# Kernel optimization log

Hardware: AMD Instinct MI355X
Metric: run time of the kernel (lower is better)

Reference implementation:

```python
import jax, jax.numpy as jnp
import numpy as np
from jax import lax

N, L = 4000, 128          # total sentences, sentence length
VOCAB = 50002             # 50000 words + unk + blk
VEC_DIM, POS_DIM = 50, 5
EMB = VEC_DIM + 2 * POS_DIM   # 60
HID = 230
NPOS = 201                # 2*max_pos_length+1
NBAG, BAGSZ = 500, 8
NREL = 25


def setup_inputs() -> dict:
    key = jax.random.key(0)
    ks = jax.random.split(key, 10)
    X = jax.random.randint(ks[0], (N, L), 0, 50000)
    pos1 = jax.random.randint(ks[1], (N, L), 0, NPOS)
    pos2 = jax.random.randint(ks[2], (N, L), 0, NPOS)
    mask = jnp.zeros((N, L), dtype=jnp.int64)       # unused by CNN encoder
    length = jnp.full((N,), L, dtype=jnp.int64)     # unused by CNN encoder
    starts = jnp.arange(NBAG) * BAGSZ
    scope = jnp.stack([starts, starts + BAGSZ], axis=1)  # [NBAG, 2] contiguous bags
    relation = jax.random.randint(ks[3], (NBAG,), 0, NREL)
    word_emb = jax.random.normal(ks[4], (VOCAB, VEC_DIM), jnp.float32) * 0.1
    pos1_emb = jax.random.normal(ks[5], (NPOS, POS_DIM), jnp.float32) * 0.1
    pos2_emb = jax.random.normal(ks[6], (NPOS, POS_DIM), jnp.float32) * 0.1
    conv_w = jax.random.normal(ks[7], (HID, EMB, 3), jnp.float32) * (1.0 / np.sqrt(EMB * 3))
    conv_b = jnp.zeros((HID,), jnp.float32)
    rel_w = jax.random.normal(ks[8], (NREL, HID), jnp.float32) * (1.0 / np.sqrt(HID))
    rel_b = jnp.zeros((NREL,), jnp.float32)
    return {"X": X, "pos1": pos1, "pos2": pos2, "mask": mask, "length": length,
            "scope": scope, "relation": relation, "word_emb": word_emb,
            "pos1_emb": pos1_emb, "pos2_emb": pos2_emb, "conv_w": conv_w,
            "conv_b": conv_b, "rel_w": rel_w, "rel_b": rel_b}


def reference(X, pos1, pos2, mask, length, scope, relation,
              word_emb, pos1_emb, pos2_emb, conv_w, conv_b, rel_w, rel_b):
    # --- word_pos_embedding: gather + concat -> [N, L, EMB]
    emb = jnp.concatenate([word_emb[X], pos1_emb[pos1], pos2_emb[pos2]], axis=-1)
    # --- CNN encoder: conv1d(k=3, same pad) -> max-pool over seq -> relu
    h = lax.conv_general_dilated(
        emb.transpose(0, 2, 1), conv_w, window_strides=(1,), padding='SAME',
        dimension_numbers=('NCH', 'OIH', 'NCH'))  # [N, HID, L]
    h = jax.nn.relu(jnp.max(h + conv_b[None, :, None], axis=2))  # [N, HID]
    # (dropout p=0.0 -> identity)
    # --- ragged per-bag softmax attention pooling (training path, relation given)
    sizes = scope[:, 1] - scope[:, 0]
    bag_ids = jnp.repeat(jnp.arange(NBAG), sizes, total_repeat_length=N)  # [N]
    rel_q = rel_w[relation]                       # [NBAG, HID] attention queries
    logits = jnp.sum(h * rel_q[bag_ids], axis=-1)  # [N]
    m = jax.ops.segment_max(logits, bag_ids, num_segments=NBAG)
    e = jnp.exp(logits - m[bag_ids])
    denom = jax.ops.segment_sum(e, bag_ids, num_segments=NBAG)
    alpha = e / denom[bag_ids]                     # per-bag softmax weights
    bag_rep = jax.ops.segment_sum(alpha[:, None] * h, bag_ids, num_segments=NBAG)  # [NBAG, HID]
    # --- relation classifier
    return bag_rep @ rel_w.T + rel_b               # [NBAG, NREL]
```

## Files before the change

### kernel.cpp

```cpp
#include <hip/hip_runtime.h>
#include <hip/hip_bf16.h>

#define NSENT 4000
#define LSEQ  128
#define VEC   50
#define POS   5
#define EMBD  60
#define HIDD  230
#define HSTR  232
#define NBAG  500
#define NREL  25
#define NTILEP 16
#define KSTEPS 6
#define ESTR  72
#define SLOTS 130
#define SSTR  (SLOTS * ESTR)

typedef __attribute__((ext_vector_type(8))) short short8;
typedef __attribute__((ext_vector_type(4))) float f32x4;

__device__ __forceinline__ unsigned short f2bf(float f) {
    union { float f; unsigned u; } v; v.f = f;
    unsigned u = v.u + 0x7FFF + ((v.u >> 16) & 1);
    return (unsigned short)(u >> 16);
}

__device__ __forceinline__ unsigned pk(float a, float b) {
    __hip_bfloat162 h = __float22bfloat162_rn(float2{a, b});
    union { __hip_bfloat162 h; unsigned u; } c; c.h = h;
    return c.u;
}

__global__ __launch_bounds__(256) void prep_b(const float* __restrict__ conv_w,
                                              unsigned short* __restrict__ Bfrag) {
    int idx = blockIdx.x * 256 + threadIdx.x;
    if (idx >= NTILEP * KSTEPS * 64 * 8) return;
    int j    = idx & 7;
    int lane = (idx >> 3) & 63;
    int t    = idx >> 9;
    int ks   = t % KSTEPS;
    int nt   = t / KSTEPS;
    int c    = nt * 16 + (lane & 15);
    int klin = ks * 32 + (lane >> 4) * 8 + j;
    int tap  = klin >> 6;
    int e    = klin & 63;
    float v  = 0.f;
    if (c < HIDD) {
        int eidx = -1;
        if (e < 50)                 eidx = e;
        else if (e >= 52 && e < 56) eidx = 50 + (e - 52);
        else if (e >= 56 && e < 60) eidx = 55 + (e - 56);
        else if (e == 60)           eidx = 54;
        else if (e == 62)           eidx = 59;
        if (eidx >= 0) v = conv_w[(c * EMBD + eidx) * 3 + tap];
    }
    Bfrag[idx] = f2bf(v);
}

__global__ __launch_bounds__(512, 4) void encoder(
    const int*   __restrict__ X,  const int* __restrict__ P1, const int* __restrict__ P2,
    const float* __restrict__ wemb, const float* __restrict__ p1emb, const float* __restrict__ p2emb,
    const unsigned short* __restrict__ Bfrag, const float* __restrict__ conv_b,
    float* __restrict__ H)
{
    __shared__ unsigned short embS[2 * SSTR];
    __shared__ int xS[2 * LSEQ], p1S[2 * LSEQ], p2S[2 * LSEQ];
    const int b2 = blockIdx.x * 2, tid = threadIdx.x;
    const int lane = tid & 63;
    const int wave = __builtin_amdgcn_readfirstlane(tid >> 6);
    const int nt0  = wave * 2;
    const int m    = lane & 15;
    const int quad = lane >> 4;

    short8 Bw[2][KSTEPS];
    #pragma unroll
    for (int t = 0; t < 2; ++t)
        #pragma unroll
        for (int ks = 0; ks < KSTEPS; ++ks)
            Bw[t][ks] = *(const short8*)(Bfrag + ((size_t)((nt0 + t) * KSTEPS + ks) * 64 + lane) * 8);

    #pragma unroll
    for (int it = 0; it < 2; ++it) {
        int i = tid + it * 512;
        if (i < 768) {
            int which = i >> 8, l2 = i & 255;
            const int* src = (which == 0) ? X : (which == 1) ? P1 : P2;
            int v = src[(size_t)b2 * LSEQ + l2];
            int* dst = (which == 0) ? xS : (which == 1) ? p1S : p2S;
            dst[l2] = v;
        } else {
            int t = i - 768;
            if (t < 128) {
                int sent = t >> 6;
                int r = (t & 32) ? (SLOTS - 1) : 0;
                *(unsigned*)(embS + sent * SSTR + r * ESTR + (t & 31) * 2) = 0u;
            }
        }
    }
    __syncthreads();

    #pragma unroll
    for (int it = 0; it < (2 * LSEQ * 16) / 512; ++it) {
        int i = tid + it * 512;
        int sent = i >> 11, rem = i & 2047;
        int l = rem >> 4, j = rem & 15;
        int li = sent * LSEQ + l;
        unsigned short* dst = embS + sent * SSTR + (l + 1) * ESTR;
        uint2 v;
        if (j < 13) {
            const float* src = wemb + (size_t)xS[li] * VEC + j * 4;
            float2 fa = *(const float2*)(src);
            float a2 = 0.f, a3 = 0.f;
            if (j < 12) { float2 fb = *(const float2*)(src + 2); a2 = fb.x; a3 = fb.y; }
            v.x = pk(fa.x, fa.y); v.y = pk(a2, a3);
        } else if (j == 13) {
            const float* p = p1emb + p1S[li] * POS;
            v.x = pk(p[0], p[1]); v.y = pk(p[2], p[3]);
        } else if (j == 14) {
            const float* p = p2emb + p2S[li] * POS;
            v.x = pk(p[0], p[1]); v.y = pk(p[2], p[3]);
        } else {
            float a = p1emb[p1S[li] * POS + 4];
            float b = p2emb[p2S[li] * POS + 4];
            v.x = pk(a, 0.f); v.y = pk(b, 0.f);
        }
        *(uint2*)(dst + (j < 13 ? j * 4 : 52 + (j - 13) * 4)) = v;
    }
    __syncthreads();

    #pragma unroll 1
    for (int s = 0; s < 2; ++s) {
        const unsigned short* eb = embS + s * SSTR;
        float maxv[2][4];
        #pragma unroll
        for (int t = 0; t < 2; ++t)
            #pragma unroll
            for (int r = 0; r < 4; ++r) maxv[t][r] = -1e30f;

        #pragma unroll
        for (int mt = 0; mt < 8; ++mt) {
            short8 A[KSTEPS];
            #pragma unroll
            for (int ks = 0; ks < KSTEPS; ++ks) {
                int tap = ks >> 1;
                int col = (ks & 1) * 32 + quad * 8;
                int row = mt * 16 + m + tap;
                A[ks] = *(const short8*)(eb + row * ESTR + col);
            }
            f32x4 acc[2];
            #pragma unroll
            for (int t = 0; t < 2; ++t) acc[t] = (f32x4){0.f, 0.f, 0.f, 0.f};
            #pragma unroll
            for (int ks = 0; ks < KSTEPS; ++ks)
                #pragma unroll
                for (int t = 0; t < 2; ++t)
                    acc[t] = __builtin_amdgcn_mfma_f32_16x16x32_bf16(A[ks], Bw[t][ks], acc[t], 0, 0, 0);
            #pragma unroll
            for (int t = 0; t < 2; ++t)
                #pragma unroll
                for (int r = 0; r < 4; ++r)
                    maxv[t][r] = fmaxf(maxv[t][r], acc[t][r]);
        }

        #pragma unroll
        for (int t = 0; t < 2; ++t) {
            float v = fmaxf(fmaxf(maxv[t][0], maxv[t][1]),
                            fmaxf(maxv[t][2], maxv[t][3]));
            v = fmaxf(v, __shfl_xor(v, 16));
            v = fmaxf(v, __shfl_xor(v, 32));
            int c = (nt0 + t) * 16 + lane;
            if (lane < 16 && c < HIDD)
                H[(size_t)(b2 + s) * HSTR + c] = fmaxf(v + conv_b[c], 0.f);
        }
    }
}

__global__ __launch_bounds__(64) void attn(
    const float* __restrict__ H, const float* __restrict__ rel_w, const float* __restrict__ rel_b,
    const int* __restrict__ relation, const int* __restrict__ scope,
    float* __restrict__ out)
{
    const int b = blockIdx.x, lane = threadIdx.x;
    const int start = scope[2 * b];
    int ns = scope[2 * b + 1] - start;
    if (ns > 8) ns = 8;
    const int rel = relation[b];

    float q[4], h[8][4];
    #pragma unroll
    for (int k = 0; k < 4; ++k) {
        int c = lane + 64 * k;
        q[k] = (c < HIDD) ? rel_w[rel * HIDD + c] : 0.f;
    }
    #pragma unroll
    for (int s = 0; s < 8; ++s)
        #pragma unroll
        for (int k = 0; k < 4; ++k) {
            int c = lane + 64 * k;
            h[s][k] = (s < ns && c < HIDD) ? H[(size_t)(start + s) * HSTR + c] : 0.f;
        }

    float logit[8];
    #pragma unroll
    for (int s = 0; s < 8; ++s) {
        float t = q[0] * h[s][0] + q[1] * h[s][1] + q[2] * h[s][2] + q[3] * h[s][3];
        #pragma unroll
        for (int off = 32; off > 0; off >>= 1) t += __shfl_xor(t, off);
        logit[s] = t;
    }

    float mx = -1e30f;
    for (int s = 0; s < ns; ++s) mx = fmaxf(mx, logit[s]);
    float a[8], den = 0.f;
    #pragma unroll
    for (int s = 0; s < 8; ++s) { a[s] = (s < ns) ? expf(logit[s] - mx) : 0.f; den += a[s]; }
    float inv = 1.f / den;

    float rep[4];
    #pragma unroll
    for (int k = 0; k < 4; ++k) {
        float r = 0.f;
        #pragma unroll
        for (int s = 0; s < 8; ++s) r += a[s] * h[s][k];
        rep[k] = r * inv;
    }

    #pragma unroll 5
    for (int g = 0; g < NREL; ++g) {
        float t = 0.f;
        #pragma unroll
        for (int k = 0; k < 4; ++k) {
            int c = lane + 64 * k;
            t += (c < HIDD) ? rel_w[g * HIDD + c] * rep[k] : 0.f;
        }
        #pragma unroll
        for (int off = 32; off > 0; off >>= 1) t += __shfl_xor(t, off);
        if (lane == 0) out[b * NREL + g] = t + rel_b[g];
    }
}

extern "C" void kernel_launch(void* const* d_in, const int* in_sizes, int n_in,
                              void* d_out, int out_size, void* d_ws, size_t ws_size,
                              hipStream_t stream) {
    const int*   X        = (const int*)d_in[0];
    const int*   P1       = (const int*)d_in[1];
    const int*   P2       = (const int*)d_in[2];
    const int*   scope    = (const int*)d_in[5];
    const int*   relation = (const int*)d_in[6];
    const float* wemb     = (const float*)d_in[7];
    const float* p1emb    = (const float*)d_in[8];
    const float* p2emb    = (const float*)d_in[9];
    const float* conv_w   = (const float*)d_in[10];
    const float* conv_b   = (const float*)d_in[11];
    const float* rel_w    = (const float*)d_in[12];
    const float* rel_b    = (const float*)d_in[13];

    char* ws = (char*)d_ws;
    float* H = (float*)ws;
    size_t off = (size_t)NSENT * HSTR * 4;
    unsigned short* Bfrag = (unsigned short*)(ws + off);

    const int btot = NTILEP * KSTEPS * 64 * 8;
    hipLaunchKernelGGL(prep_b, dim3((btot + 255) / 256), dim3(256), 0, stream,
                       conv_w, Bfrag);
    hipLaunchKernelGGL(encoder, dim3(NSENT / 2), dim3(512), 0, stream,
                       X, P1, P2, wemb, p1emb, p2emb, Bfrag, conv_b, H);
    hipLaunchKernelGGL(attn, dim3(NBAG), dim3(64), 0, stream,
                       H, rel_w, rel_b, relation, scope, (float*)d_out);
}
```

Baseline: 183.2 us.

## Process one sentence per encoder block and drop index staging in LDS

The encoder now gives each block a single sentence instead of two, doubling the grid to one block per sentence and halving the LDS embedding buffer. Token and position indices are read straight from global memory inside the gather loop, which removes the separate index-staging phase and one barrier. The aim is more parallelism and occupancy with less serial work per block. In exchange, each block reloads the conv weight fragments for half as many sentences, so weight-load overhead per sentence doubles.

```diff
diff --git a/kernel.cpp b/kernel.cpp
--- a/kernel.cpp
+++ b/kernel.cpp
@@ -63,9 +63,8 @@
     const unsigned short* __restrict__ Bfrag, const float* __restrict__ conv_b,
     float* __restrict__ H)
 {
-    __shared__ unsigned short embS[2 * SSTR];
-    __shared__ int xS[2 * LSEQ], p1S[2 * LSEQ], p2S[2 * LSEQ];
-    const int b2 = blockIdx.x * 2, tid = threadIdx.x;
+    __shared__ unsigned short embS[SSTR];
+    const int b = blockIdx.x, tid = threadIdx.x;
     const int lane = tid & 63;
     const int wave = __builtin_amdgcn_readfirstlane(tid >> 6);
     const int nt0  = wave * 2;
@@ -79,99 +78,79 @@
         for (int ks = 0; ks < KSTEPS; ++ks)
             Bw[t][ks] = *(const short8*)(Bfrag + ((size_t)((nt0 + t) * KSTEPS + ks) * 64 + lane) * 8);
 
-    #pragma unroll
-    for (int it = 0; it < 2; ++it) {
+    if (tid < 64) {
+        int r = (tid & 32) ? (SLOTS - 1) : 0;
+        *(unsigned*)(embS + r * ESTR + (tid & 31) * 2) = 0u;
+    }
+
+    #pragma unroll
+    for (int it = 0; it < (LSEQ * 16) / 512; ++it) {
         int i = tid + it * 512;
-        if (i < 768) {
-            int which = i >> 8, l2 = i & 255;
-            const int* src = (which == 0) ? X : (which == 1) ? P1 : P2;
-            int v = src[(size_t)b2 * LSEQ + l2];
-            int* dst = (which == 0) ? xS : (which == 1) ? p1S : p2S;
-            dst[l2] = v;
-        } else {
-            int t = i - 768;
-            if (t < 128) {
-                int sent = t >> 6;
-                int r = (t & 32) ? (SLOTS - 1) : 0;
-                *(unsigned*)(embS + sent * SSTR + r * ESTR + (t & 31) * 2) = 0u;
-            }
-        }
-    }
-    __syncthreads();
-
-    #pragma unroll
-    for (int it = 0; it < (2 * LSEQ * 16) / 512; ++it) {
-        int i = tid + it * 512;
-        int sent = i >> 11, rem = i & 2047;
-        int l = rem >> 4, j = rem & 15;
-        int li = sent * LSEQ + l;
-        unsigned short* dst = embS + sent * SSTR + (l + 1) * ESTR;
+        int l = i >> 4, j = i & 15;
+        size_t tb = (size_t)b * LSEQ + l;
+        unsigned short* dst = embS + (l + 1) * ESTR;
         uint2 v;
         if (j < 13) {
-            const float* src = wemb + (size_t)xS[li] * VEC + j * 4;
+            const float* src = wemb + (size_t)X[tb] * VEC + j * 4;
             float2 fa = *(const float2*)(src);
             float a2 = 0.f, a3 = 0.f;
             if (j < 12) { float2 fb = *(const float2*)(src + 2); a2 = fb.x; a3 = fb.y; }
             v.x = pk(fa.x, fa.y); v.y = pk(a2, a3);
         } else if (j == 13) {
-            const float* p = p1emb + p1S[li] * POS;
+            const float* p = p1emb + P1[tb] * POS;
             v.x = pk(p[0], p[1]); v.y = pk(p[2], p[3]);
         } else if (j == 14) {
-            const float* p = p2emb + p2S[li] * POS;
+            const float* p = p2emb + P2[tb] * POS;
             v.x = pk(p[0], p[1]); v.y = pk(p[2], p[3]);
         } else {
-            float a = p1emb[p1S[li] * POS + 4];
-            float b = p2emb[p2S[li] * POS + 4];
-            v.x = pk(a, 0.f); v.y = pk(b, 0.f);
+            float a  = p1emb[P1[tb] * POS + 4];
+            float b2 = p2emb[P2[tb] * POS + 4];
+            v.x = pk(a, 0.f); v.y = pk(b2, 0.f);
         }
         *(uint2*)(dst + (j < 13 ? j * 4 : 52 + (j - 13) * 4)) = v;
     }
     __syncthreads();
 
-    #pragma unroll 1
-    for (int s = 0; s < 2; ++s) {
-        const unsigned short* eb = embS + s * SSTR;
-        float maxv[2][4];
+    float maxv[2][4];
+    #pragma unroll
+    for (int t = 0; t < 2; ++t)
+        #pragma unroll
+        for (int r = 0; r < 4; ++r) maxv[t][r] = -1e30f;
+
+    #pragma unroll
+    for (int mt = 0; mt < 8; ++mt) {
+        short8 A[KSTEPS];
+        #pragma unroll
+        for (int ks = 0; ks < KSTEPS; ++ks) {
+            int tap = ks >> 1;
+            int col = (ks & 1) * 32 + quad * 8;
+            int row = mt * 16 + m + tap;
+            A[ks] = *(const short8*)(embS + row * ESTR + col);
+        }
+        f32x4 acc[2];
+        #pragma unroll
+        for (int t = 0; t < 2; ++t) acc[t] = (f32x4){0.f, 0.f, 0.f, 0.f};
+        #pragma unroll
+        for (int ks = 0; ks < KSTEPS; ++ks)
+            #pragma unroll
+            for (int t = 0; t < 2; ++t)
+                acc[t] = __builtin_amdgcn_mfma_f32_16x16x32_bf16(A[ks], Bw[t][ks], acc[t], 0, 0, 0);
         #pragma unroll
         for (int t = 0; t < 2; ++t)
             #pragma unroll
-            for (int r = 0; r < 4; ++r) maxv[t][r] = -1e30f;
-
-        #pragma unroll
-        for (int mt = 0; mt < 8; ++mt) {
-            short8 A[KSTEPS];
-            #pragma unroll
-            for (int ks = 0; ks < KSTEPS; ++ks) {
-                int tap = ks >> 1;
-                int col = (ks & 1) * 32 + quad * 8;
-                int row = mt * 16 + m + tap;
-                A[ks] = *(const short8*)(eb + row * ESTR + col);
-            }
-            f32x4 acc[2];
-            #pragma unroll
-            for (int t = 0; t < 2; ++t) acc[t] = (f32x4){0.f, 0.f, 0.f, 0.f};
-            #pragma unroll
-            for (int ks = 0; ks < KSTEPS; ++ks)
-                #pragma unroll
-                for (int t = 0; t < 2; ++t)
-                    acc[t] = __builtin_amdgcn_mfma_f32_16x16x32_bf16(A[ks], Bw[t][ks], acc[t], 0, 0, 0);
-            #pragma unroll
-            for (int t = 0; t < 2; ++t)
-                #pragma unroll
-                for (int r = 0; r < 4; ++r)
-                    maxv[t][r] = fmaxf(maxv[t][r], acc[t][r]);
-        }
-
-        #pragma unroll
-        for (int t = 0; t < 2; ++t) {
-            float v = fmaxf(fmaxf(maxv[t][0], maxv[t][1]),
-                            fmaxf(maxv[t][2], maxv[t][3]));
-            v = fmaxf(v, __shfl_xor(v, 16));
-            v = fmaxf(v, __shfl_xor(v, 32));
-            int c = (nt0 + t) * 16 + lane;
-            if (lane < 16 && c < HIDD)
-                H[(size_t)(b2 + s) * HSTR + c] = fmaxf(v + conv_b[c], 0.f);
-        }
+            for (int r = 0; r < 4; ++r)
+                maxv[t][r] = fmaxf(maxv[t][r], acc[t][r]);
+    }
+
+    #pragma unroll
+    for (int t = 0; t < 2; ++t) {
+        float v = fmaxf(fmaxf(maxv[t][0], maxv[t][1]),
+                        fmaxf(maxv[t][2], maxv[t][3]));
+        v = fmaxf(v, __shfl_xor(v, 16));
+        v = fmaxf(v, __shfl_xor(v, 32));
+        int c = (nt0 + t) * 16 + lane;
+        if (lane < 16 && c < HIDD)
+            H[(size_t)b * HSTR + c] = fmaxf(v + conv_b[c], 0.f);
     }
 }
 
@@ -263,7 +242,7 @@
     const int btot = NTILEP * KSTEPS * 64 * 8;
     hipLaunchKernelGGL(prep_b, dim3((btot + 255) / 256), dim3(256), 0, stream,
                        conv_w, Bfrag);
-    hipLaunchKernelGGL(encoder, dim3(NSENT / 2), dim3(512), 0, stream,
+    hipLaunchKernelGGL(encoder, dim3(NSENT), dim3(512), 0, stream,
                        X, P1, P2, wemb, p1emb, p2emb, Bfrag, conv_b, H);
     hipLaunchKernelGGL(attn, dim3(NBAG), dim3(64), 0, stream,
                        H, rel_w, rel_b, relation, scope, (float*)d_out);
```

Result: slower. 209.9 us (+14.6%).

## Split embedding gather into separate kernel writing bf16 slab for conv

Applied to the files above, without the earlier changes.

Splits the fused encoder into an embed kernel, which gathers word and position embeddings into a padded bf16 slab in global memory, and a conv kernel that bulk-copies the slab into LDS before running the MFMA convolution and max-pool. The aim is to keep the scattered gather latency out of the MFMA kernel and give the gather its own higher-parallelism launch. In exchange it adds an extra launch and a global round trip of about 75 MB, and the slab path runs only when the workspace is large enough, with the fused kernel kept as a fallback.

```diff
diff --git a/kernel.cpp b/kernel.cpp
--- a/kernel.cpp
+++ b/kernel.cpp
@@ -57,7 +57,125 @@
     Bfrag[idx] = f2bf(v);
 }
 
-__global__ __launch_bounds__(512, 4) void encoder(
+__global__ __launch_bounds__(256) void embed(
+    const int*   __restrict__ X,  const int* __restrict__ P1, const int* __restrict__ P2,
+    const float* __restrict__ wemb, const float* __restrict__ p1emb, const float* __restrict__ p2emb,
+    unsigned short* __restrict__ slab)
+{
+    const int snt = blockIdx.x, tid = threadIdx.x;
+    unsigned short* base = slab + (size_t)snt * SSTR;
+
+    if (tid < 64) {
+        int r = (tid & 32) ? (SLOTS - 1) : 0;
+        *(unsigned*)(base + r * ESTR + (tid & 31) * 2) = 0u;
+    }
+
+    #pragma unroll
+    for (int it = 0; it < (LSEQ * 16) / 256; ++it) {
+        int i = tid + it * 256;
+        int l = i >> 4, j = i & 15;
+        size_t tb = (size_t)snt * LSEQ + l;
+        unsigned short* dst = base + (l + 1) * ESTR;
+        uint2 v;
+        if (j < 13) {
+            const float* src = wemb + (size_t)X[tb] * VEC + j * 4;
+            float2 fa = *(const float2*)(src);
+            float a2 = 0.f, a3 = 0.f;
+            if (j < 12) { float2 fb = *(const float2*)(src + 2); a2 = fb.x; a3 = fb.y; }
+            v.x = pk(fa.x, fa.y); v.y = pk(a2, a3);
+        } else if (j == 13) {
+            const float* p = p1emb + P1[tb] * POS;
+            v.x = pk(p[0], p[1]); v.y = pk(p[2], p[3]);
+        } else if (j == 14) {
+            const float* p = p2emb + P2[tb] * POS;
+            v.x = pk(p[0], p[1]); v.y = pk(p[2], p[3]);
+        } else {
+            float a  = p1emb[P1[tb] * POS + 4];
+            float b2 = p2emb[P2[tb] * POS + 4];
+            v.x = pk(a, 0.f); v.y = pk(b2, 0.f);
+        }
+        *(uint2*)(dst + (j < 13 ? j * 4 : 52 + (j - 13) * 4)) = v;
+    }
+}
+
+__global__ __launch_bounds__(512, 4) void conv_enc(
+    const unsigned short* __restrict__ slab,
+    const unsigned short* __restrict__ Bfrag, const float* __restrict__ conv_b,
+    float* __restrict__ H)
+{
+    __shared__ unsigned short embS[20480];
+    const int b2 = blockIdx.x * 2, tid = threadIdx.x;
+    const int lane = tid & 63;
+    const int wave = __builtin_amdgcn_readfirstlane(tid >> 6);
+    const int nt0  = wave * 2;
+    const int m    = lane & 15;
+    const int quad = lane >> 4;
+
+    const uint4* src = (const uint4*)(slab + (size_t)b2 * SSTR);
+    uint4 tmp[5];
+    #pragma unroll
+    for (int it = 0; it < 5; ++it) tmp[it] = src[tid + it * 512];
+    #pragma unroll
+    for (int it = 0; it < 5; ++it) *(uint4*)(embS + (size_t)(tid + it * 512) * 8) = tmp[it];
+    __builtin_amdgcn_sched_barrier(0);
+
+    short8 Bw[2][KSTEPS];
+    #pragma unroll
+    for (int t = 0; t < 2; ++t)
+        #pragma unroll
+        for (int ks = 0; ks < KSTEPS; ++ks)
+            Bw[t][ks] = *(const short8*)(Bfrag + ((size_t)((nt0 + t) * KSTEPS + ks) * 64 + lane) * 8);
+
+    __syncthreads();
+
+    #pragma unroll 1
+    for (int s = 0; s < 2; ++s) {
+        const unsigned short* eb = embS + s * SSTR;
+        float maxv[2][4];
+        #pragma unroll
+        for (int t = 0; t < 2; ++t)
+            #pragma unroll
+            for (int r = 0; r < 4; ++r) maxv[t][r] = -1e30f;
+
+        #pragma unroll
+        for (int mt = 0; mt < 8; ++mt) {
+            short8 A[KSTEPS];
+            #pragma unroll
+            for (int ks = 0; ks < KSTEPS; ++ks) {
+                int tap = ks >> 1;
+                int col = (ks & 1) * 32 + quad * 8;
+                int row = mt * 16 + m + tap;
+                A[ks] = *(const short8*)(eb + row * ESTR + col);
+            }
+            f32x4 acc[2];
+            #pragma unroll
+            for (int t = 0; t < 2; ++t) acc[t] = (f32x4){0.f, 0.f, 0.f, 0.f};
+            #pragma unroll
+            for (int ks = 0; ks < KSTEPS; ++ks)
+                #pragma unroll
+                for (int t = 0; t < 2; ++t)
+                    acc[t] = __builtin_amdgcn_mfma_f32_16x16x32_bf16(A[ks], Bw[t][ks], acc[t], 0, 0, 0);
+            #pragma unroll
+            for (int t = 0; t < 2; ++t)
+                #pragma unroll
+                for (int r = 0; r < 4; ++r)
+                    maxv[t][r] = fmaxf(maxv[t][r], acc[t][r]);
+        }
+
+        #pragma unroll
+        for (int t = 0; t < 2; ++t) {
+            float v = fmaxf(fmaxf(maxv[t][0], maxv[t][1]),
+                            fmaxf(maxv[t][2], maxv[t][3]));
+            v = fmaxf(v, __shfl_xor(v, 16));
+            v = fmaxf(v, __shfl_xor(v, 32));
+            int c = (nt0 + t) * 16 + lane;
+            if (lane < 16 && c < HIDD)
+                H[(size_t)(b2 + s) * HSTR + c] = fmaxf(v + conv_b[c], 0.f);
+        }
+    }
+}
+
+__global__ __launch_bounds__(512, 4) void encoder_fused(
     const int*   __restrict__ X,  const int* __restrict__ P1, const int* __restrict__ P2,
     const float* __restrict__ wemb, const float* __restrict__ p1emb, const float* __restrict__ p2emb,
     const unsigned short* __restrict__ Bfrag, const float* __restrict__ conv_b,
@@ -257,14 +375,24 @@
 
     char* ws = (char*)d_ws;
     float* H = (float*)ws;
-    size_t off = (size_t)NSENT * HSTR * 4;
-    unsigned short* Bfrag = (unsigned short*)(ws + off);
+    const size_t offB = (size_t)NSENT * HSTR * 4;
+    unsigned short* Bfrag = (unsigned short*)(ws + offB);
+    const size_t offS = offB + (size_t)NTILEP * KSTEPS * 64 * 8 * 2;
+    unsigned short* slab = (unsigned short*)(ws + offS);
+    const size_t need = offS + (size_t)NSENT * SSTR * 2 + 4096;
 
     const int btot = NTILEP * KSTEPS * 64 * 8;
     hipLaunchKernelGGL(prep_b, dim3((btot + 255) / 256), dim3(256), 0, stream,
                        conv_w, Bfrag);
-    hipLaunchKernelGGL(encoder, dim3(NSENT / 2), dim3(512), 0, stream,
-                       X, P1, P2, wemb, p1emb, p2emb, Bfrag, conv_b, H);
+    if (ws_size >= need) {
+        hipLaunchKernelGGL(embed, dim3(NSENT), dim3(256), 0, stream,
+                           X, P1, P2, wemb, p1emb, p2emb, slab);
+        hipLaunchKernelGGL(conv_enc, dim3(NSENT / 2), dim3(512), 0, stream,
+                           slab, Bfrag, conv_b, H);
+    } else {
+        hipLaunchKernelGGL(encoder_fused, dim3(NSENT / 2), dim3(512), 0, stream,
+                           X, P1, P2, wemb, p1emb, p2emb, Bfrag, conv_b, H);
+    }
     hipLaunchKernelGGL(attn, dim3(NBAG), dim3(64), 0, stream,
                        H, rel_w, rel_b, relation, scope, (float*)d_out);
 }
```

After: 196.6 us. 1.07x slower.
